# Kernel optimization log

Measured on AMD Instinct MI355X. Metric: run time of the kernel, lower is better.

## Reference

```python
import jax, jax.numpy as jnp
import numpy as np

S, B, D, H, HD = 2048, 4, 1280, 16, 80  # seq, batch, d_model, heads, head_dim
NSEG = 8


def setup_inputs() -> dict:
    key = jax.random.key(0)
    k0, k1, k2 = jax.random.split(key, 3)
    x = jax.random.normal(k0, (S, B, D), dtype=jnp.float32)
    Wqkv = jax.random.normal(k1, (D, 3 * D), dtype=jnp.float32) * 0.02
    bqkv = jnp.zeros((3 * D,), dtype=jnp.float32)
    Wproj = jax.random.normal(k2, (D, 4 * D), dtype=jnp.float32) * 0.02
    bproj = jnp.zeros((4 * D,), dtype=jnp.float32)
    # 8 equal windows of 256 tokens: [0, 256, 512, ..., 2048]
    cu_seqlens = (jnp.arange(NSEG + 1, dtype=jnp.int32) * (S // NSEG))
    return {"x": x, "Wqkv": Wqkv, "bqkv": bqkv, "Wproj": Wproj,
            "bproj": bproj, "cu_seqlens": cu_seqlens}


def reference(x, Wqkv, bqkv, Wproj, bproj, cu_seqlens):
    s, b, d = x.shape
    qkv = x @ Wqkv + bqkv                     # [s, b, 3d]
    q, k, v = jnp.split(qkv, 3, axis=2)       # each [s, b, d]
    def to_bhsd(t):
        return t.reshape(s, b, H, HD).transpose(1, 2, 0, 3)  # [b, h, s, hd]
    q, k, v = to_bhsd(q), to_bhsd(k), to_bhsd(v)
    # Block-diagonal mask: token t belongs to window searchsorted(cu[1:], t, right)
    pos = jnp.arange(s)
    seg = jnp.searchsorted(cu_seqlens[1:], pos, side='right')  # [s]
    bias = jnp.where(seg[:, None] == seg[None, :], 0.0,
                     jnp.finfo(x.dtype).min)                   # [s, s]
    scale = 1.0 / jnp.sqrt(jnp.asarray(HD, dtype=x.dtype))
    scores = jnp.einsum('bhsd,bhtd->bhst', q, k) * scale + bias
    attn = jax.nn.softmax(scores, axis=-1)
    out = jnp.einsum('bhst,bhtd->bhsd', attn, v)               # [b, h, s, hd]
    context = out.transpose(2, 0, 1, 3).reshape(s, b, H * HD)  # [s, b, d]
    return context @ Wproj + bproj                             # [s, b, 4d]
```

## Files before the change

kernel.cpp:

```cpp
#include <hip/hip_runtime.h>

typedef _Float16 f16;
typedef _Float16 f16x8 __attribute__((ext_vector_type(8)));
typedef _Float16 f16x4 __attribute__((ext_vector_type(4)));
typedef float    f32x4 __attribute__((ext_vector_type(4)));
typedef unsigned int u32t;

#define AS1 __attribute__((address_space(1)))
#define AS3 __attribute__((address_space(3)))

static __device__ __forceinline__ void gload_lds16(const void* g, void* l) {
  __builtin_amdgcn_global_load_lds((const AS1 u32t*)g, (AS3 u32t*)l, 16, 0, 0);
}

static __device__ __forceinline__ f16x8 zero8() {
  f16x8 z;
#pragma unroll
  for (int j = 0; j < 8; ++j) z[j] = (f16)0;
  return z;
}

__global__ void k_cvt_x(const float* __restrict__ in, f16* __restrict__ out, int n4) {
  int stride = gridDim.x * blockDim.x;
  for (int i = blockIdx.x * blockDim.x + threadIdx.x; i < n4; i += stride) {
    float4 v = ((const float4*)in)[i];
    f16x4 o;
    o[0] = (f16)v.x; o[1] = (f16)v.y; o[2] = (f16)v.z; o[3] = (f16)v.w;
    ((f16x4*)out)[i] = o;
  }
}

__global__ void k_cvt_w_t(const float* __restrict__ W, f16* __restrict__ Wt, int N) {
  __shared__ float T[32][33];
  int bk = blockIdx.x % 40;
  int bn = blockIdx.x / 40;
  int k0 = bk * 32, n0 = bn * 32;
  int r = threadIdx.x >> 5;
  int c = threadIdx.x & 31;
#pragma unroll
  for (int i = 0; i < 4; ++i)
    T[r + i * 8][c] = W[(size_t)(k0 + r + i * 8) * N + n0 + c];
  __syncthreads();
#pragma unroll
  for (int i = 0; i < 4; ++i)
    Wt[(size_t)(n0 + r + i * 8) * 1280 + k0 + c] = (f16)T[c][r + i * 8];
}

template<int NCOLS, bool F16OUT>
__global__ __launch_bounds__(512, 1)
void gemm_nt256(const f16* __restrict__ A, const f16* __restrict__ Bt,
                const float* __restrict__ bias, void* __restrict__ Cout)
{
  __shared__ __align__(16) char lds[131072];
  const int tid = threadIdx.x;
  const int wave = tid >> 6, lane = tid & 63;
  const int rl = lane & 15, g = lane >> 4;
  const int wm = wave >> 2, wn = wave & 3;

  constexpr int NBN = NCOLS / 256;
  constexpr int NWG = 32 * NBN;
  const int bid = blockIdx.x;
  const int wgid = (bid & 7) * (NWG / 8) + (bid >> 3);
  const int bm = wgid / NBN, bn = wgid % NBN;
  const long row0 = (long)bm * 256, col0 = (long)bn * 256;

  const int subA = wave * 8 + (lane >> 3);
  const int cpA  = (((lane & 7) ^ (subA & 7)) << 4);
  const char* gAt = (const char*)A + (row0 + subA) * 2560 + cpA;
  const int subB = (wave & 3) * 8 + (lane >> 3);
  const int cpB  = (((lane & 7) ^ (subB & 7)) << 4);
  const char* gBt = (const char*)Bt + (col0 + (wave >> 2) * 64 + subB) * 2560 + cpB;
  char* const dA = lds + wave * 1024;
  char* const dB = lds + 65536 + wave * 1024;

  auto STA = [&](int mh, int buf, int kb) {
#pragma unroll
    for (int l = 0; l < 2; ++l)
      gload_lds16(gAt + mh * (64 * 2560) + l * (128 * 2560) + kb,
                  dA + buf * 32768 + mh * 16384 + l * 8192);
  };
  auto STB = [&](int nh, int buf, int kb) {
#pragma unroll
    for (int l = 0; l < 2; ++l)
      gload_lds16(gBt + nh * (32 * 2560) + l * (128 * 2560) + kb,
                  dB + buf * 32768 + nh * 16384 + l * 8192);
  };

  const int swz0 = ((0 + g) ^ (rl & 7)) << 4;
  const int swz1 = ((4 + g) ^ (rl & 7)) << 4;
  const int aro = wm * 8192 + rl * 128;
  const int bro = 65536 + wn * 4096 + rl * 128;

  auto LDA = [&](f16x8 (&af)[8], int buf, int mh) {
#pragma unroll
    for (int m = 0; m < 4; ++m) {
      const char* p = lds + buf * 32768 + mh * 16384 + aro + m * 2048;
      af[m * 2 + 0] = *(const f16x8*)(p + swz0);
      af[m * 2 + 1] = *(const f16x8*)(p + swz1);
    }
  };
  auto LDB = [&](f16x8 (&bf)[4], int buf, int nh) {
#pragma unroll
    for (int n = 0; n < 2; ++n) {
      const char* p = lds + buf * 32768 + nh * 16384 + bro + n * 2048;
      bf[n * 2 + 0] = *(const f16x8*)(p + swz0);
      bf[n * 2 + 1] = *(const f16x8*)(p + swz1);
    }
  };

  f32x4 acc[8][4];
#pragma unroll
  for (int m = 0; m < 8; ++m)
#pragma unroll
    for (int n = 0; n < 4; ++n) acc[m][n] = (f32x4){0.f, 0.f, 0.f, 0.f};

  auto MM = [&](int mh, int nh, const f16x8 (&af)[8], const f16x8 (&bf)[4]) {
    __builtin_amdgcn_s_setprio(1);
#pragma unroll
    for (int m = 0; m < 4; ++m)
#pragma unroll
      for (int n = 0; n < 2; ++n)
#pragma unroll
        for (int kk = 0; kk < 2; ++kk)
          acc[mh * 4 + m][nh * 2 + n] = __builtin_amdgcn_mfma_f32_16x16x32_f16(
              af[m * 2 + kk], bf[n * 2 + kk], acc[mh * 4 + m][nh * 2 + n], 0, 0, 0);
    __builtin_amdgcn_s_setprio(0);
  };

#define BAR()   do { __builtin_amdgcn_s_barrier(); asm volatile("" ::: "memory"); } while (0)
#define WLGKM() asm volatile("s_waitcnt lgkmcnt(0)" ::: "memory")
#define WVM(N)  asm volatile("s_waitcnt vmcnt(" #N ")" ::: "memory")

  auto TILE = [&](int buf, int kbB1, int kbN, int mode) {
    f16x8 af[8], bf0[4], bf1[4];
    LDA(af, buf, 0); LDB(bf0, buf, 0);
    if (mode <= 1) STB(1, buf ^ 1, kbB1);
    BAR(); WLGKM(); MM(0, 0, af, bf0); BAR();
    LDB(bf1, buf, 1);
    if (mode == 0) STA(0, buf, kbN);
    BAR(); WLGKM(); MM(0, 1, af, bf1); BAR();
    LDA(af, buf, 1);
    if (mode == 0) STB(0, buf, kbN);
    BAR(); WLGKM(); MM(1, 1, af, bf1); BAR();
    if (mode == 0) STA(1, buf, kbN);
    if (mode == 0) { WVM(6); } else if (mode == 1) { WVM(0); }
    BAR(); MM(1, 0, af, bf0);
    if (mode != 2) BAR();
  };

  STA(0, 0, 0); STB(0, 0, 0); STA(1, 0, 0); STB(1, 0, 0);
  STA(0, 1, 128); STB(0, 1, 128); STA(1, 1, 128);
  WVM(6); BAR();

#pragma unroll 1
  for (int it = 0; it < 9; ++it) {
    const int kb = it * 256;
    TILE(0, kb + 128, kb + 256, 0);
    TILE(1, kb + 256, kb + 384, 0);
  }
  TILE(0, 2432, 0, 1);
  TILE(1, 0, 0, 2);

#undef BAR
#undef WLGKM
#undef WVM

#pragma unroll
  for (int m = 0; m < 8; ++m) {
#pragma unroll
    for (int n = 0; n < 4; ++n) {
      long c = col0 + wn * 64 + n * 16 + rl;
      float bv = bias[c];
#pragma unroll
      for (int r = 0; r < 4; ++r) {
        long rr = row0 + wm * 128 + m * 16 + g * 4 + r;
        float v = acc[m][n][r] + bv;
        if (F16OUT) ((f16*)Cout)[rr * NCOLS + c] = (f16)v;
        else        ((float*)Cout)[rr * NCOLS + c] = v;
      }
    }
  }
}

template<int NCOLS>
__global__ __launch_bounds__(256, 2)
void gemm_nt128(const f16* __restrict__ A, const f16* __restrict__ Bt,
                const float* __restrict__ bias, float* __restrict__ Cout)
{
  __shared__ __align__(16) char lds[32768];
  f16* const sA = (f16*)lds;
  f16* const sB = (f16*)(lds + 16384);
  const int tid = threadIdx.x;
  const int wave = tid >> 6, lane = tid & 63;
  constexpr int NBN = NCOLS / 128;
  const int bm = blockIdx.x / NBN, bn = blockIdx.x % NBN;
  const long row0 = (long)bm * 128, col0 = (long)bn * 128;

  f32x4 acc[4][4];
#pragma unroll
  for (int i = 0; i < 4; ++i)
#pragma unroll
    for (int j = 0; j < 4; ++j) acc[i][j] = (f32x4){0.f, 0.f, 0.f, 0.f};

  const int wr = (wave >> 1) * 64, wc = (wave & 1) * 64;

  int segr[4], segoff[4];
#pragma unroll
  for (int i = 0; i < 4; ++i) {
    int o = (wave * 4 + i) * 1024 + lane * 16;
    int r = o >> 7, cb = o & 127;
    segr[i] = r;
    segoff[i] = cb ^ ((r & 7) << 4);
  }

  const char* Ab = (const char*)A;
  const char* Bb = (const char*)Bt;

  for (int kt = 0; kt < 20; ++kt) {
    __syncthreads();
#pragma unroll
    for (int i = 0; i < 4; ++i) {
      const char* ga = Ab + ((row0 + segr[i]) * 1280 + kt * 64) * 2 + segoff[i];
      gload_lds16(ga, (char*)sA + (wave * 4 + i) * 1024);
      const char* gb = Bb + ((col0 + segr[i]) * 1280 + kt * 64) * 2 + segoff[i];
      gload_lds16(gb, (char*)sB + (wave * 4 + i) * 1024);
    }
    __syncthreads();

#pragma unroll
    for (int kk = 0; kk < 2; ++kk) {
      const int rl = lane & 15, g = lane >> 4, x7 = lane & 7;
      const int ph = (kk * 4 + g) ^ x7;
      f16x8 af[4], bf[4];
#pragma unroll
      for (int mt = 0; mt < 4; ++mt)
        af[mt] = *(const f16x8*)(sA + (wr + mt * 16 + rl) * 64 + ph * 8);
#pragma unroll
      for (int nt = 0; nt < 4; ++nt)
        bf[nt] = *(const f16x8*)(sB + (wc + nt * 16 + rl) * 64 + ph * 8);
#pragma unroll
      for (int mt = 0; mt < 4; ++mt)
#pragma unroll
        for (int nt = 0; nt < 4; ++nt)
          acc[mt][nt] = __builtin_amdgcn_mfma_f32_16x16x32_f16(af[mt], bf[nt], acc[mt][nt], 0, 0, 0);
    }
  }

  {
    float* bb = (float*)lds;
    const int rl = lane & 15, g = lane >> 4;
    const int wm = wave >> 1;
    const int lrow = tid >> 2, q = tid & 3;
#pragma unroll
    for (int p = 0; p < 2; ++p) {
      __syncthreads();
#pragma unroll
      for (int mt2 = 0; mt2 < 2; ++mt2) {
        int mt = p * 2 + mt2;
#pragma unroll
        for (int nt = 0; nt < 4; ++nt) {
          int col = wc + nt * 16 + rl;
          float bv = bias[col0 + col];
#pragma unroll
          for (int r = 0; r < 4; ++r) {
            int clrow = wm * 32 + mt2 * 16 + g * 4 + r;
            bb[clrow * 128 + (col ^ ((clrow & 7) << 2))] = acc[mt][nt][r] + bv;
          }
        }
      }
      __syncthreads();
      long grow = row0 + (lrow >> 5) * 64 + p * 32 + (lrow & 31);
      float* gout = Cout + grow * NCOLS + col0;
#pragma unroll
      for (int j = 0; j < 8; ++j) {
        int col = j * 16 + q * 4;
        f32x4 v = *(const f32x4*)(bb + lrow * 128 + (col ^ ((lrow & 7) << 2)));
        *(f32x4*)(gout + col) = v;
      }
    }
  }
}

__global__ void k_vt(const f16* __restrict__ qkv, f16* __restrict__ vt) {
  __shared__ __align__(16) f16 T[128 * 136];
  int bid = blockIdx.x;
  int sc16 = bid & 15, bh = bid >> 4;
  int b = bh >> 4, h = bh & 15;
  int s0 = sc16 * 128;
  int t = threadIdx.x;
#pragma unroll
  for (int i = 0; i < 5; ++i) {
    int cid = i * 256 + t;
    int s = cid / 10, c = cid % 10;
    const f16* g = qkv + (size_t)((s0 + s) * 4 + b) * 3840 + 2560 + h * 80 + c * 8;
    f16x8 v = *(const f16x8*)g;
    int phys = c ^ ((s >> 3) & 7);
    *(f16x8*)(T + s * 136 + phys * 8) = v;
  }
  __syncthreads();
#pragma unroll
  for (int i = 0; i < 5; ++i) {
    int oid = i * 256 + t;
    int sc8 = oid & 15, hd = oid >> 4;
    f16x8 o;
#pragma unroll
    for (int j = 0; j < 8; ++j) {
      int row = sc8 * 8 + j;
      int phys = (hd >> 3) ^ (sc8 & 7);
      o[j] = T[row * 136 + phys * 8 + (hd & 7)];
    }
    *(f16x8*)(vt + (size_t)(bh * 80 + hd) * 2048 + s0 + sc8 * 8) = o;
  }
}

__global__ __launch_bounds__(512, 2)
void k_attn(const f16* __restrict__ qkv, const f16* __restrict__ vt,
            f16* __restrict__ ctx)
{
  __shared__ __align__(16) f16 sK[256 * 104];
  __shared__ __align__(16) f16 sV[80 * 264];
  __shared__ __align__(16) f16 sP[256 * 72];

  const int bid = blockIdx.x;
  const int seg = bid & 7, h = (bid >> 3) & 15, b = bid >> 7;
  const int t = threadIdx.x;
  const int wave = t >> 6, lane = t & 63;
  const int s_key0 = seg * 256;

#pragma unroll
  for (int i = 0; i < 5; ++i) {
    int cid = i * 512 + t;
    int key = cid / 10, c = cid % 10;
    const f16* g = qkv + (size_t)((s_key0 + key) * 4 + b) * 3840 + 1280 + h * 80 + c * 8;
    *(f16x8*)(sK + key * 104 + c * 8) = *(const f16x8*)g;
  }
  {
    int key = t >> 1, c = t & 1;
    *(f16x8*)(sK + key * 104 + 80 + c * 8) = zero8();
  }
#pragma unroll
  for (int i = 0; i < 5; ++i) {
    int cid = i * 512 + t;
    int hd = cid >> 5, c = cid & 31;
    const f16* g = vt + (size_t)((b * 16 + h) * 80 + hd) * 2048 + s_key0 + c * 8;
    *(f16x8*)(sV + hd * 264 + c * 8) = *(const f16x8*)g;
  }

  const int q0 = s_key0 + wave * 32;
  const int rl = lane & 15, g = lane >> 4;
  f16x8 qfl[3], qfh[3];
  {
    const f16* gl = qkv + (size_t)((q0 + rl) * 4 + b) * 3840 + h * 80;
    const f16* gh = qkv + (size_t)((q0 + 16 + rl) * 4 + b) * 3840 + h * 80;
    qfl[0] = *(const f16x8*)(gl + g * 8);
    qfh[0] = *(const f16x8*)(gh + g * 8);
    qfl[1] = *(const f16x8*)(gl + 32 + g * 8);
    qfh[1] = *(const f16x8*)(gh + 32 + g * 8);
    if (g < 2) { qfl[2] = *(const f16x8*)(gl + 64 + g * 8); qfh[2] = *(const f16x8*)(gh + 64 + g * 8); }
    else       { qfl[2] = zero8(); qfh[2] = zero8(); }
  }
  __syncthreads();

  f32x4 scl[16], sch[16];
#pragma unroll
  for (int nt = 0; nt < 16; ++nt) { scl[nt] = (f32x4){0.f,0.f,0.f,0.f}; sch[nt] = (f32x4){0.f,0.f,0.f,0.f}; }
#pragma unroll
  for (int nt = 0; nt < 16; ++nt) {
#pragma unroll
    for (int kk = 0; kk < 3; ++kk) {
      f16x8 bf = *(const f16x8*)(sK + (nt * 16 + rl) * 104 + kk * 32 + g * 8);
      scl[nt] = __builtin_amdgcn_mfma_f32_16x16x32_f16(qfl[kk], bf, scl[nt], 0, 0, 0);
      sch[nt] = __builtin_amdgcn_mfma_f32_16x16x32_f16(qfh[kk], bf, sch[nt], 0, 0, 0);
    }
  }

  const float scale = 0.11180339887498949f;
  float invl[4], invh[4];
#pragma unroll
  for (int r = 0; r < 4; ++r) {
    float ml = -1e30f, mh = -1e30f;
#pragma unroll
    for (int nt = 0; nt < 16; ++nt) { ml = fmaxf(ml, scl[nt][r]); mh = fmaxf(mh, sch[nt][r]); }
#pragma unroll
    for (int off = 8; off >= 1; off >>= 1) { ml = fmaxf(ml, __shfl_xor(ml, off)); mh = fmaxf(mh, __shfl_xor(mh, off)); }
    ml *= scale; mh *= scale;
    float suml = 0.f, sumh = 0.f;
#pragma unroll
    for (int nt = 0; nt < 16; ++nt) {
      float pl = __expf(scl[nt][r] * scale - ml);
      float ph = __expf(sch[nt][r] * scale - mh);
      scl[nt][r] = pl; sch[nt][r] = ph;
      suml += pl; sumh += ph;
    }
#pragma unroll
    for (int off = 8; off >= 1; off >>= 1) { suml += __shfl_xor(suml, off); sumh += __shfl_xor(sumh, off); }
    invl[r] = 1.0f / suml; invh[r] = 1.0f / sumh;
  }

  f32x4 ol[5], oh[5];
#pragma unroll
  for (int nt = 0; nt < 5; ++nt) { ol[nt] = (f32x4){0.f,0.f,0.f,0.f}; oh[nt] = (f32x4){0.f,0.f,0.f,0.f}; }
  const int prow0 = wave * 32;
  for (int ch = 0; ch < 4; ++ch) {
#pragma unroll
    for (int f = 0; f < 4; ++f) {
      int nt = ch * 4 + f;
#pragma unroll
      for (int r = 0; r < 4; ++r) {
        sP[(prow0 + g * 4 + r) * 72 + f * 16 + rl]      = (f16)scl[nt][r];
        sP[(prow0 + 16 + g * 4 + r) * 72 + f * 16 + rl] = (f16)sch[nt][r];
      }
    }
#pragma unroll
    for (int kk = 0; kk < 2; ++kk) {
      f16x8 pal = *(const f16x8*)(sP + (prow0 + rl) * 72 + kk * 32 + g * 8);
      f16x8 pah = *(const f16x8*)(sP + (prow0 + 16 + rl) * 72 + kk * 32 + g * 8);
#pragma unroll
      for (int nt = 0; nt < 5; ++nt) {
        f16x8 vb = *(const f16x8*)(sV + (nt * 16 + rl) * 264 + ch * 64 + kk * 32 + g * 8);
        ol[nt] = __builtin_amdgcn_mfma_f32_16x16x32_f16(pal, vb, ol[nt], 0, 0, 0);
        oh[nt] = __builtin_amdgcn_mfma_f32_16x16x32_f16(pah, vb, oh[nt], 0, 0, 0);
      }
    }
  }

#pragma unroll
  for (int nt = 0; nt < 5; ++nt) {
    int hd = nt * 16 + rl;
#pragma unroll
    for (int r = 0; r < 4; ++r) {
      long qrl = q0 + g * 4 + r;
      ctx[(qrl * 4 + b) * 1280 + h * 80 + hd] = (f16)(ol[nt][r] * invl[r]);
      long qrh = q0 + 16 + g * 4 + r;
      ctx[(qrh * 4 + b) * 1280 + h * 80 + hd] = (f16)(oh[nt][r] * invh[r]);
    }
  }
}

extern "C" void kernel_launch(void* const* d_in, const int* in_sizes, int n_in,
                              void* d_out, int out_size, void* d_ws, size_t ws_size,
                              hipStream_t stream)
{
  const float* x     = (const float*)d_in[0];
  const float* Wqkv  = (const float*)d_in[1];
  const float* bqkv  = (const float*)d_in[2];
  const float* Wproj = (const float*)d_in[3];
  const float* bproj = (const float*)d_in[4];

  char* ws = (char*)d_ws;
  f16* X16   = (f16*)(ws);
  f16* WQT   = (f16*)(ws + 20971520);
  f16* WPT   = (f16*)(ws + 30801920);
  f16* QKV16 = (f16*)(ws + 43909120);
  f16* VT    = (f16*)(ws + 106823680);
  f16* CTX16 = X16;

  k_cvt_x<<<4096, 256, 0, stream>>>(x, X16, 8192 * 1280 / 4);
  k_cvt_w_t<<<40 * 120, 256, 0, stream>>>(Wqkv, WQT, 3840);
  k_cvt_w_t<<<40 * 160, 256, 0, stream>>>(Wproj, WPT, 5120);
  gemm_nt256<3840, true><<<480, 512, 0, stream>>>(X16, WQT, bqkv, QKV16);
  k_vt<<<1024, 256, 0, stream>>>(QKV16, VT);
  k_attn<<<512, 512, 0, stream>>>(QKV16, VT, CTX16);
  gemm_nt128<5120><<<64 * 40, 256, 0, stream>>>(CTX16, WPT, bproj, (float*)d_out);
}
```

Measured before the change: 258.5 us.

## Merge prep kernels, raise proj GEMM occupancy, store epilogue directly

Merges the three conversion kernels (x cast and the two weight transposes) into one launch, which removes two launch gaps. Raises the projection GEMM's launch bounds from 2 to 4 blocks per CU. Replaces its LDS-staged, coalesced float4 epilogue with direct scalar stores from the MFMA accumulators. The direct stores drop two barriers and LDS traffic but write a large fp32 output in partially coalesced 4-byte chunks, and the tighter launch bounds may force register spills.

```diff
diff --git a/kernel.cpp b/kernel.cpp
--- a/kernel.cpp
+++ b/kernel.cpp
@@ -20,30 +20,37 @@
   return z;
 }
 
-__global__ void k_cvt_x(const float* __restrict__ in, f16* __restrict__ out, int n4) {
-  int stride = gridDim.x * blockDim.x;
-  for (int i = blockIdx.x * blockDim.x + threadIdx.x; i < n4; i += stride) {
-    float4 v = ((const float4*)in)[i];
-    f16x4 o;
-    o[0] = (f16)v.x; o[1] = (f16)v.y; o[2] = (f16)v.z; o[3] = (f16)v.w;
-    ((f16x4*)out)[i] = o;
-  }
-}
-
-__global__ void k_cvt_w_t(const float* __restrict__ W, f16* __restrict__ Wt, int N) {
+__global__ void k_prep(const float* __restrict__ x,
+                       const float* __restrict__ Wqkv,
+                       const float* __restrict__ Wproj,
+                       f16* __restrict__ X16, f16* __restrict__ WQT,
+                       f16* __restrict__ WPT)
+{
   __shared__ float T[32][33];
-  int bk = blockIdx.x % 40;
-  int bn = blockIdx.x / 40;
-  int k0 = bk * 32, n0 = bn * 32;
-  int r = threadIdx.x >> 5;
-  int c = threadIdx.x & 31;
-#pragma unroll
-  for (int i = 0; i < 4; ++i)
-    T[r + i * 8][c] = W[(size_t)(k0 + r + i * 8) * N + n0 + c];
-  __syncthreads();
-#pragma unroll
-  for (int i = 0; i < 4; ++i)
-    Wt[(size_t)(n0 + r + i * 8) * 1280 + k0 + c] = (f16)T[c][r + i * 8];
+  const int bid = blockIdx.x;
+  if (bid < 11200) {
+    const float* W; f16* Wt; int N; int b2;
+    if (bid < 4800) { W = Wqkv;  Wt = WQT; N = 3840; b2 = bid; }
+    else            { W = Wproj; Wt = WPT; N = 5120; b2 = bid - 4800; }
+    int bk = b2 % 40, bn = b2 / 40;
+    int k0 = bk * 32, n0 = bn * 32;
+    int r = threadIdx.x >> 5, c = threadIdx.x & 31;
+#pragma unroll
+    for (int i = 0; i < 4; ++i)
+      T[r + i * 8][c] = W[(size_t)(k0 + r + i * 8) * N + n0 + c];
+    __syncthreads();
+#pragma unroll
+    for (int i = 0; i < 4; ++i)
+      Wt[(size_t)(n0 + r + i * 8) * 1280 + k0 + c] = (f16)T[c][r + i * 8];
+  } else {
+    const int n4 = 8192 * 1280 / 4;
+    for (int i = (bid - 11200) * 256 + threadIdx.x; i < n4; i += 2048 * 256) {
+      float4 v = ((const float4*)x)[i];
+      f16x4 o;
+      o[0] = (f16)v.x; o[1] = (f16)v.y; o[2] = (f16)v.z; o[3] = (f16)v.w;
+      ((f16x4*)X16)[i] = o;
+    }
+  }
 }
 
 template<int NCOLS, bool F16OUT>
@@ -183,7 +190,7 @@
 }
 
 template<int NCOLS>
-__global__ __launch_bounds__(256, 2)
+__global__ __launch_bounds__(256, 4)
 void gemm_nt128(const f16* __restrict__ A, const f16* __restrict__ Bt,
                 const float* __restrict__ bias, float* __restrict__ Cout)
 {
@@ -246,36 +253,17 @@
     }
   }
 
-  {
-    float* bb = (float*)lds;
-    const int rl = lane & 15, g = lane >> 4;
-    const int wm = wave >> 1;
-    const int lrow = tid >> 2, q = tid & 3;
-#pragma unroll
-    for (int p = 0; p < 2; ++p) {
-      __syncthreads();
-#pragma unroll
-      for (int mt2 = 0; mt2 < 2; ++mt2) {
-        int mt = p * 2 + mt2;
-#pragma unroll
-        for (int nt = 0; nt < 4; ++nt) {
-          int col = wc + nt * 16 + rl;
-          float bv = bias[col0 + col];
-#pragma unroll
-          for (int r = 0; r < 4; ++r) {
-            int clrow = wm * 32 + mt2 * 16 + g * 4 + r;
-            bb[clrow * 128 + (col ^ ((clrow & 7) << 2))] = acc[mt][nt][r] + bv;
-          }
-        }
-      }
-      __syncthreads();
-      long grow = row0 + (lrow >> 5) * 64 + p * 32 + (lrow & 31);
-      float* gout = Cout + grow * NCOLS + col0;
-#pragma unroll
-      for (int j = 0; j < 8; ++j) {
-        int col = j * 16 + q * 4;
-        f32x4 v = *(const f32x4*)(bb + lrow * 128 + (col ^ ((lrow & 7) << 2)));
-        *(f32x4*)(gout + col) = v;
+  const int rl = lane & 15, g = lane >> 4;
+#pragma unroll
+  for (int mt = 0; mt < 4; ++mt) {
+#pragma unroll
+    for (int nt = 0; nt < 4; ++nt) {
+      long c = col0 + wc + nt * 16 + rl;
+      float bv = bias[c];
+#pragma unroll
+      for (int r = 0; r < 4; ++r) {
+        long rr = row0 + wr + mt * 16 + g * 4 + r;
+        Cout[rr * NCOLS + c] = acc[mt][nt][r] + bv;
       }
     }
   }
@@ -455,9 +443,7 @@
   f16* VT    = (f16*)(ws + 106823680);
   f16* CTX16 = X16;
 
-  k_cvt_x<<<4096, 256, 0, stream>>>(x, X16, 8192 * 1280 / 4);
-  k_cvt_w_t<<<40 * 120, 256, 0, stream>>>(Wqkv, WQT, 3840);
-  k_cvt_w_t<<<40 * 160, 256, 0, stream>>>(Wproj, WPT, 5120);
+  k_prep<<<13248, 256, 0, stream>>>(x, Wqkv, Wproj, X16, WQT, WPT);
   gemm_nt256<3840, true><<<480, 512, 0, stream>>>(X16, WQT, bqkv, QKV16);
   k_vt<<<1024, 256, 0, stream>>>(QKV16, VT);
   k_attn<<<512, 512, 0, stream>>>(QKV16, VT, CTX16);
```

After: 253.3 us. -2.0%, faster.
